# Kernel tuning notes

Measured on AMD Instinct MI355X. Metric: run time of the kernel, lower is better.

## Reference

```python
import jax, jax.numpy as jnp
import numpy as np

NUM_HEADS = 16
D_MODEL = 1024
DEPTH = D_MODEL // NUM_HEADS
B, S = 4, 1024  # q,k seq len = S; v seq len = S-1


def setup_inputs() -> dict:
    key = jax.random.key(0)
    ks = jax.random.split(key, 6)
    scale = 1.0 / np.sqrt(D_MODEL)
    return {
        "v": jax.random.normal(ks[0], (B, S - 1, D_MODEL), dtype=jnp.float32),
        "k": jax.random.normal(ks[1], (B, S, D_MODEL), dtype=jnp.float32),
        "q": jax.random.normal(ks[2], (B, S, D_MODEL), dtype=jnp.float32),
        "mask": jnp.zeros((B, S - 1, S - 1), dtype=jnp.float32),
        "Wv": jax.random.normal(ks[3], (D_MODEL, D_MODEL), dtype=jnp.float32) * scale,
        "bv": jnp.zeros((D_MODEL,), dtype=jnp.float32),
        "Wd": jax.random.normal(ks[4], (D_MODEL, D_MODEL), dtype=jnp.float32) * scale,
        "bd": jnp.zeros((D_MODEL,), dtype=jnp.float32),
    }


def _split_heads(x):
    # (B, T, d_model) -> (B, H, T, depth)
    b, t, _ = x.shape
    return x.reshape(b, t, NUM_HEADS, DEPTH).transpose(0, 2, 1, 3)


def reference(v, k, q, mask, Wv, bv, Wd, bd):
    # 3-D q/k path: qq=q, kk=k (q_layers/k_layers/wq/wk unused)
    vv = v @ Wv + bv                       # (B, S-1, d_model)
    qh = _split_heads(q)                   # (B, H, S, depth)
    kh = _split_heads(k)                   # (B, H, S, depth)
    vh = _split_heads(vv)                  # (B, H, S-1, depth)

    scores = jnp.einsum('bhqd,bhkd->bhqk', qh, kh)      # (B, H, S, S)
    scores = scores[:, :, 1:, :-1]                      # (B, H, S-1, S-1)
    dk = jnp.asarray(DEPTH, scores.dtype)
    nl = jax.nn.relu(scores / jnp.sqrt(dk))
    nl = nl + mask[:, None, :, :] * (-1e9)
    att = jax.nn.softmax(nl, axis=-1)                   # (B, H, S-1, S-1)

    out = jnp.einsum('bhqk,bhkd->bhqd', att, vh)        # (B, H, S-1, depth)
    out = out.transpose(0, 2, 1, 3).reshape(v.shape[0], -1, D_MODEL)  # (B, S-1, d_model)
    output = out @ Wd + bd
    return output, att
```

## Files before the change

### kernel.cpp

```cpp
#include <hip/hip_runtime.h>
#include <hip/hip_bf16.h>

#define NUM_HEADS 16
#define DM 1024
#define DEPTH 64
#define BB 4
#define SS 1024
#define SL 1023
#define M_ROWS (BB*SL)

typedef __attribute__((ext_vector_type(8))) short short8;
typedef __attribute__((ext_vector_type(4))) float floatx4;

__device__ inline unsigned short f2bf(float f) {
  __hip_bfloat16 hb = __float2bfloat16(f);
  return *reinterpret_cast<unsigned short*>(&hb);
}
__device__ inline short8 ld_frag(const unsigned short* p) {
  return *reinterpret_cast<const short8*>(p);
}

#define GLDS(g, l) __builtin_amdgcn_global_load_lds( \
    (const __attribute__((address_space(1))) void*)(g), \
    (__attribute__((address_space(3))) void*)(l), 16, 0, 0)

__global__ __launch_bounds__(256) void f32_to_bf16_vec(
    const float* __restrict__ in, unsigned short* __restrict__ out, int n8)
{
  int i = blockIdx.x * 256 + threadIdx.x;
  if (i >= n8) return;
  const float4 f0 = ((const float4*)in)[(size_t)i * 2];
  const float4 f1 = ((const float4*)in)[(size_t)i * 2 + 1];
  unsigned short t[8];
  t[0]=f2bf(f0.x); t[1]=f2bf(f0.y); t[2]=f2bf(f0.z); t[3]=f2bf(f0.w);
  t[4]=f2bf(f1.x); t[5]=f2bf(f1.y); t[6]=f2bf(f1.z); t[7]=f2bf(f1.w);
  ((uint4*)out)[i] = *(uint4*)t;
}

__global__ __launch_bounds__(256) void transpose_to_bf16(
    const float* __restrict__ W, unsigned short* __restrict__ WT)
{
  __shared__ unsigned short tile[64][72];
  const int tid = threadIdx.x;
  const int k0 = blockIdx.y * 64, n0 = blockIdx.x * 64;
  {
    const int kl = tid >> 2, nc = (tid & 3) * 16;
    const float* src = W + (size_t)(k0 + kl) * DM + n0 + nc;
    #pragma unroll
    for (int j = 0; j < 16; j += 4) {
      float4 f = *(const float4*)(src + j);
      tile[nc + j + 0][kl] = f2bf(f.x);
      tile[nc + j + 1][kl] = f2bf(f.y);
      tile[nc + j + 2][kl] = f2bf(f.z);
      tile[nc + j + 3][kl] = f2bf(f.w);
    }
  }
  __syncthreads();
  {
    const int nl = tid >> 2, kc = (tid & 3) * 16;
    unsigned short tmp[16];
    #pragma unroll
    for (int j = 0; j < 16; j++) tmp[j] = tile[nl][kc + j];
    unsigned short* dst = WT + (size_t)(n0 + nl) * DM + k0 + kc;
    *(uint4*)&dst[0] = *(uint4*)&tmp[0];
    *(uint4*)&dst[8] = *(uint4*)&tmp[8];
  }
}

template <bool OUT_BF16>
__global__ __launch_bounds__(256) void gemm_bt(
    const unsigned short* __restrict__ A,
    const unsigned short* __restrict__ BT,
    const float* __restrict__ bias,
    void* __restrict__ Cv, int M)
{
  constexpr int BM = 64, BN = 128, BK = 32;
  __shared__ __align__(16) unsigned short As[2][BM * BK];
  __shared__ __align__(16) unsigned short Bs[2][BN * BK];

  const int tid = threadIdx.x;
  const int w = tid >> 6, lane = tid & 63, q4 = lane >> 4, l16 = lane & 15;
  const int wm = w >> 1, wn = w & 1;
  const int rb = blockIdx.y * BM;
  const int cb = blockIdx.x * BN;

  const int a_row = tid >> 2;
  const int a_slot = (tid & 3) ^ ((a_row >> 1) & 3);
  int a_grow = rb + a_row; if (a_grow >= M) a_grow = M - 1;
  const unsigned short* a_src = A + (size_t)a_grow * DM + a_slot * 8;
  const int b_row0 = tid >> 2;
  const int b_row1 = 64 + (tid >> 2);
  const int b_slot0 = (tid & 3) ^ ((b_row0 >> 1) & 3);
  const int b_slot1 = (tid & 3) ^ ((b_row1 >> 1) & 3);
  const unsigned short* b_src0 = BT + (size_t)(cb + b_row0) * DM + b_slot0 * 8;
  const unsigned short* b_src1 = BT + (size_t)(cb + b_row1) * DM + b_slot1 * 8;

  int aoff[2], boff[4];
  #pragma unroll
  for (int i = 0; i < 2; i++) {
    int r = wm * 32 + i * 16 + l16;
    aoff[i] = r * BK + ((q4 ^ ((r >> 1) & 3)) * 8);
  }
  #pragma unroll
  for (int j = 0; j < 4; j++) {
    int r = wn * 64 + j * 16 + l16;
    boff[j] = r * BK + ((q4 ^ ((r >> 1) & 3)) * 8);
  }

  floatx4 acc[2][4];
  #pragma unroll
  for (int i = 0; i < 2; i++)
    #pragma unroll
    for (int j = 0; j < 4; j++) acc[i][j] = (floatx4){0.f,0.f,0.f,0.f};

  GLDS(a_src,  &As[0][tid * 8]);
  GLDS(b_src0, &Bs[0][tid * 8]);
  GLDS(b_src1, &Bs[0][2048 + tid * 8]);
  __syncthreads();

  int cur = 0;
  constexpr int NT = DM / BK;
  for (int t = 0; t < NT; ++t) {
    if (t + 1 < NT) {
      const int kn = (t + 1) * BK;
      GLDS(a_src + kn,  &As[cur ^ 1][tid * 8]);
      GLDS(b_src0 + kn, &Bs[cur ^ 1][tid * 8]);
      GLDS(b_src1 + kn, &Bs[cur ^ 1][2048 + tid * 8]);
    }
    short8 af[2], bfr[4];
    #pragma unroll
    for (int i = 0; i < 2; i++) af[i] = ld_frag(&As[cur][aoff[i]]);
    #pragma unroll
    for (int j = 0; j < 4; j++) bfr[j] = ld_frag(&Bs[cur][boff[j]]);
    #pragma unroll
    for (int i = 0; i < 2; i++)
      #pragma unroll
      for (int j = 0; j < 4; j++)
        acc[i][j] = __builtin_amdgcn_mfma_f32_16x16x32_bf16(af[i], bfr[j], acc[i][j], 0, 0, 0);
    __syncthreads();
    cur ^= 1;
  }

  #pragma unroll
  for (int j = 0; j < 4; j++) {
    int col = cb + wn * 64 + j * 16 + l16;
    float bb = bias[col];
    #pragma unroll
    for (int i = 0; i < 2; i++) {
      #pragma unroll
      for (int r = 0; r < 4; r++) {
        int m = rb + wm * 32 + i * 16 + q4 * 4 + r;
        if (m < M) {
          float val = acc[i][j][r] + bb;
          if (OUT_BF16) ((unsigned short*)Cv)[(size_t)m * DM + col] = f2bf(val);
          else          ((float*)Cv)[(size_t)m * DM + col] = val;
        }
      }
    }
  }
}

__global__ __launch_bounds__(256) void attn_kernel(
    const float* __restrict__ Q, const float* __restrict__ Kg,
    const float* __restrict__ Mask, const unsigned short* __restrict__ VV,
    float* __restrict__ Att, unsigned short* __restrict__ Out2)
{
  const int qt = blockIdx.x, h = blockIdx.y, b = blockIdx.z;
  const int tid = threadIdx.x;
  const int w = tid >> 6, lane = tid & 63, q4 = lane >> 4, l16 = lane & 15;
  const int qi0 = qt * 64;
  const int qb = w * 16;

  __shared__ unsigned short qsh[64][72];
  __shared__ unsigned short ksh[64][72];
  __shared__ unsigned short vshT[64][72];
  __shared__ unsigned short psh[4][16][72];

  {
    int qr = tid >> 2, d0 = (tid & 3) * 16;
    int qi = qi0 + qr;
    unsigned short tmp[16];
    if (qi < SL) {
      const float* src = Q + ((size_t)b * SS + qi + 1) * DM + h * DEPTH + d0;
      #pragma unroll
      for (int j = 0; j < 16; j += 4) {
        float4 f = *(const float4*)(src + j);
        tmp[j+0]=f2bf(f.x); tmp[j+1]=f2bf(f.y); tmp[j+2]=f2bf(f.z); tmp[j+3]=f2bf(f.w);
      }
    } else {
      #pragma unroll
      for (int j = 0; j < 16; j++) tmp[j] = 0;
    }
    *(uint4*)&qsh[qr][d0]     = *(uint4*)&tmp[0];
    *(uint4*)&qsh[qr][d0 + 8] = *(uint4*)&tmp[8];
  }

  auto stageK = [&](int kt) {
    int kr = tid >> 2, d0 = (tid & 3) * 16;
    int kj = kt * 64 + kr;
    unsigned short tmp[16];
    if (kj < SL) {
      const float* src = Kg + ((size_t)b * SS + kj) * DM + h * DEPTH + d0;
      #pragma unroll
      for (int j = 0; j < 16; j += 4) {
        float4 f = *(const float4*)(src + j);
        tmp[j+0]=f2bf(f.x); tmp[j+1]=f2bf(f.y); tmp[j+2]=f2bf(f.z); tmp[j+3]=f2bf(f.w);
      }
    } else {
      #pragma unroll
      for (int j = 0; j < 16; j++) tmp[j] = 0;
    }
    *(uint4*)&ksh[kr][d0]     = *(uint4*)&tmp[0];
    *(uint4*)&ksh[kr][d0 + 8] = *(uint4*)&tmp[8];
  };

  auto stageV = [&](int kt) {
    int d = tid & 63, k16 = (tid >> 6) * 16;
    unsigned short tmp[16];
    #pragma unroll
    for (int j = 0; j < 16; j++) {
      int kj = kt * 64 + k16 + j;
      tmp[j] = (kj < SL) ? VV[((size_t)b * SL + kj) * DM + h * DEPTH + d] : (unsigned short)0;
    }
    *(uint4*)&vshT[d][k16]     = *(uint4*)&tmp[0];
    *(uint4*)&vshT[d][k16 + 8] = *(uint4*)&tmp[8];
  };

  __syncthreads();

  float rsv[4] = {0.f, 0.f, 0.f, 0.f};
  for (int kt = 0; kt < 16; kt++) {
    __syncthreads();
    stageK(kt);
    __syncthreads();
    #pragma unroll
    for (int nt = 0; nt < 4; nt++) {
      floatx4 s = (floatx4){0.f,0.f,0.f,0.f};
      s = __builtin_amdgcn_mfma_f32_16x16x32_bf16(
            ld_frag(&qsh[qb + l16][q4*8]), ld_frag(&ksh[nt*16 + l16][q4*8]), s, 0,0,0);
      s = __builtin_amdgcn_mfma_f32_16x16x32_bf16(
            ld_frag(&qsh[qb + l16][32 + q4*8]), ld_frag(&ksh[nt*16 + l16][32 + q4*8]), s, 0,0,0);
      int kj = kt * 64 + nt * 16 + l16;
      bool kv = kj < SL;
      int qi_b = qi0 + qb + q4 * 4;
      const float* mp = Mask + ((size_t)b * SL + qi_b) * SL + kj;
      #pragma unroll
      for (int r = 0; r < 4; r++) {
        int qi = qi_b + r;
        float mval = (kv && qi < SL) ? mp[(size_t)r * SL] : 0.f;
        float sv = fmaxf(s[r] * 0.125f, 0.f) + mval * (-1e9f);
        float p = kv ? __expf(sv) : 0.f;
        rsv[r] += p;
      }
    }
  }
  #pragma unroll
  for (int r = 0; r < 4; r++) {
    #pragma unroll
    for (int off = 1; off < 16; off <<= 1) rsv[r] += __shfl_xor(rsv[r], off, 64);
  }
  float inv[4];
  #pragma unroll
  for (int r = 0; r < 4; r++) inv[r] = 1.f / rsv[r];

  floatx4 oacc[4];
  #pragma unroll
  for (int i = 0; i < 4; i++) oacc[i] = (floatx4){0.f,0.f,0.f,0.f};

  for (int kt = 0; kt < 16; kt++) {
    __syncthreads();
    stageK(kt);
    stageV(kt);
    __syncthreads();
    #pragma unroll
    for (int nt = 0; nt < 4; nt++) {
      floatx4 s = (floatx4){0.f,0.f,0.f,0.f};
      s = __builtin_amdgcn_mfma_f32_16x16x32_bf16(
            ld_frag(&qsh[qb + l16][q4*8]), ld_frag(&ksh[nt*16 + l16][q4*8]), s, 0,0,0);
      s = __builtin_amdgcn_mfma_f32_16x16x32_bf16(
            ld_frag(&qsh[qb + l16][32 + q4*8]), ld_frag(&ksh[nt*16 + l16][32 + q4*8]), s, 0,0,0);
      int kj = kt * 64 + nt * 16 + l16;
      bool kv = kj < SL;
      int qi_b = qi0 + qb + q4 * 4;
      const float* mp = Mask + ((size_t)b * SL + qi_b) * SL + kj;
      #pragma unroll
      for (int r = 0; r < 4; r++) {
        int qi = qi_b + r;
        bool qv = qi < SL;
        float mval = (kv && qv) ? mp[(size_t)r * SL] : 0.f;
        float sv = fmaxf(s[r] * 0.125f, 0.f) + mval * (-1e9f);
        float p = kv ? __expf(sv) : 0.f;
        float pn = p * inv[r];
        if (kv && qv)
          Att[(((size_t)(b * NUM_HEADS + h)) * SL + qi) * SL + kj] = pn;
        psh[w][q4 * 4 + r][nt * 16 + l16] = f2bf(pn);
      }
    }
    short8 pa0 = ld_frag(&psh[w][l16][q4 * 8]);
    short8 pa1 = ld_frag(&psh[w][l16][32 + q4 * 8]);
    #pragma unroll
    for (int nt2 = 0; nt2 < 4; nt2++) {
      oacc[nt2] = __builtin_amdgcn_mfma_f32_16x16x32_bf16(
                    pa0, ld_frag(&vshT[nt2*16 + l16][q4*8]), oacc[nt2], 0,0,0);
      oacc[nt2] = __builtin_amdgcn_mfma_f32_16x16x32_bf16(
                    pa1, ld_frag(&vshT[nt2*16 + l16][32 + q4*8]), oacc[nt2], 0,0,0);
    }
  }

  #pragma unroll
  for (int nt2 = 0; nt2 < 4; nt2++) {
    #pragma unroll
    for (int r = 0; r < 4; r++) {
      int qi = qi0 + qb + q4 * 4 + r;
      if (qi < SL)
        Out2[((size_t)b * SL + qi) * DM + h * DEPTH + nt2 * 16 + l16] = f2bf(oacc[nt2][r]);
    }
  }
}

extern "C" void kernel_launch(void* const* d_in, const int* in_sizes, int n_in,
                              void* d_out, int out_size, void* d_ws, size_t ws_size,
                              hipStream_t stream) {
  const float* v    = (const float*)d_in[0];
  const float* k    = (const float*)d_in[1];
  const float* q    = (const float*)d_in[2];
  const float* mask = (const float*)d_in[3];
  const float* Wv   = (const float*)d_in[4];
  const float* bv   = (const float*)d_in[5];
  const float* Wd   = (const float*)d_in[6];
  const float* bd   = (const float*)d_in[7];

  float* out = (float*)d_out;
  float* att = out + (size_t)M_ROWS * DM;
  unsigned short* vv   = (unsigned short*)d_ws;
  unsigned short* out2 = vv + (size_t)M_ROWS * DM;

  unsigned short* WvT = (unsigned short*)att;
  unsigned short* vbf = WvT + (size_t)DM * DM;
  unsigned short* WdT = vv;

  const int n8 = (M_ROWS * DM) / 8;

  f32_to_bf16_vec<<<dim3((n8 + 255) / 256), 256, 0, stream>>>(v, vbf, n8);
  transpose_to_bf16<<<dim3(16, 16), 256, 0, stream>>>(Wv, WvT);
  gemm_bt<true><<<dim3(DM/128, (M_ROWS+63)/64), 256, 0, stream>>>(vbf, WvT, bv, (void*)vv, M_ROWS);
  attn_kernel<<<dim3(16, NUM_HEADS, BB), 256, 0, stream>>>(q, k, mask, vv, att, out2);
  transpose_to_bf16<<<dim3(16, 16), 256, 0, stream>>>(Wd, WdT);
  gemm_bt<false><<<dim3(DM/128, (M_ROWS+63)/64), 256, 0, stream>>>(out2, WdT, bd, (void*)out, M_ROWS);
}
```

Baseline: 667.0 us.

## Double-buffer K in attention, XOR-swizzle LDS, widen GEMM BK, nontemporal stores

The attention kernel now preloads the Q fragments into registers and double-buffers K tiles in LDS, issuing the next tile's global loads before the current compute. Padded LDS arrays are replaced with XOR-swizzled layouts to avoid bank conflicts. The GEMM K-tile grows from 32 to 64 with a matching 8-way swizzle. The attention-probability and fp32 GEMM outputs use nontemporal stores. Together these aim to hide global latency and cut LDS conflicts, at the cost of more registers and LDS, and extra barriers in the second pass.

```diff
diff --git a/kernel.cpp b/kernel.cpp
--- a/kernel.cpp
+++ b/kernel.cpp
@@ -19,6 +19,8 @@
 __device__ inline short8 ld_frag(const unsigned short* p) {
   return *reinterpret_cast<const short8*>(p);
 }
+
+#define SWZ(row, g) (((g) ^ ((row) & 7)))
 
 #define GLDS(g, l) __builtin_amdgcn_global_load_lds( \
     (const __attribute__((address_space(1))) void*)(g), \
@@ -74,7 +76,7 @@
     const float* __restrict__ bias,
     void* __restrict__ Cv, int M)
 {
-  constexpr int BM = 64, BN = 128, BK = 32;
+  constexpr int BM = 64, BN = 128, BK = 64;
   __shared__ __align__(16) unsigned short As[2][BM * BK];
   __shared__ __align__(16) unsigned short Bs[2][BN * BK];
 
@@ -84,28 +86,32 @@
   const int rb = blockIdx.y * BM;
   const int cb = blockIdx.x * BN;
 
-  const int a_row = tid >> 2;
-  const int a_slot = (tid & 3) ^ ((a_row >> 1) & 3);
-  int a_grow = rb + a_row; if (a_grow >= M) a_grow = M - 1;
-  const unsigned short* a_src = A + (size_t)a_grow * DM + a_slot * 8;
-  const int b_row0 = tid >> 2;
-  const int b_row1 = 64 + (tid >> 2);
-  const int b_slot0 = (tid & 3) ^ ((b_row0 >> 1) & 3);
-  const int b_slot1 = (tid & 3) ^ ((b_row1 >> 1) & 3);
-  const unsigned short* b_src0 = BT + (size_t)(cb + b_row0) * DM + b_slot0 * 8;
-  const unsigned short* b_src1 = BT + (size_t)(cb + b_row1) * DM + b_slot1 * 8;
-
-  int aoff[2], boff[4];
-  #pragma unroll
-  for (int i = 0; i < 2; i++) {
-    int r = wm * 32 + i * 16 + l16;
-    aoff[i] = r * BK + ((q4 ^ ((r >> 1) & 3)) * 8);
-  }
-  #pragma unroll
-  for (int j = 0; j < 4; j++) {
-    int r = wn * 64 + j * 16 + l16;
-    boff[j] = r * BK + ((q4 ^ ((r >> 1) & 3)) * 8);
-  }
+  const int srow = tid >> 3;
+  const int lg   = (tid & 7) ^ (srow & 7);
+  int ar0 = rb + srow;       if (ar0 >= M) ar0 = M - 1;
+  int ar1 = rb + 32 + srow;  if (ar1 >= M) ar1 = M - 1;
+  const unsigned short* a_src0 = A + (size_t)ar0 * DM + lg * 8;
+  const unsigned short* a_src1 = A + (size_t)ar1 * DM + lg * 8;
+  const unsigned short* b_src0 = BT + (size_t)(cb      + srow) * DM + lg * 8;
+  const unsigned short* b_src1 = BT + (size_t)(cb + 32 + srow) * DM + lg * 8;
+  const unsigned short* b_src2 = BT + (size_t)(cb + 64 + srow) * DM + lg * 8;
+  const unsigned short* b_src3 = BT + (size_t)(cb + 96 + srow) * DM + lg * 8;
+
+  int aoff[2][2], boff[4][2];
+  #pragma unroll
+  for (int i = 0; i < 2; i++)
+    #pragma unroll
+    for (int hf = 0; hf < 2; hf++) {
+      int r = wm * 32 + i * 16 + l16;
+      aoff[i][hf] = r * BK + SWZ(r, q4 + 4 * hf) * 8;
+    }
+  #pragma unroll
+  for (int j = 0; j < 4; j++)
+    #pragma unroll
+    for (int hf = 0; hf < 2; hf++) {
+      int r = wn * 64 + j * 16 + l16;
+      boff[j][hf] = r * BK + SWZ(r, q4 + 4 * hf) * 8;
+    }
 
   floatx4 acc[2][4];
   #pragma unroll
@@ -113,9 +119,12 @@
     #pragma unroll
     for (int j = 0; j < 4; j++) acc[i][j] = (floatx4){0.f,0.f,0.f,0.f};
 
-  GLDS(a_src,  &As[0][tid * 8]);
+  GLDS(a_src0, &As[0][tid * 8]);
+  GLDS(a_src1, &As[0][2048 + tid * 8]);
   GLDS(b_src0, &Bs[0][tid * 8]);
   GLDS(b_src1, &Bs[0][2048 + tid * 8]);
+  GLDS(b_src2, &Bs[0][4096 + tid * 8]);
+  GLDS(b_src3, &Bs[0][6144 + tid * 8]);
   __syncthreads();
 
   int cur = 0;
@@ -123,20 +132,30 @@
   for (int t = 0; t < NT; ++t) {
     if (t + 1 < NT) {
       const int kn = (t + 1) * BK;
-      GLDS(a_src + kn,  &As[cur ^ 1][tid * 8]);
+      GLDS(a_src0 + kn, &As[cur ^ 1][tid * 8]);
+      GLDS(a_src1 + kn, &As[cur ^ 1][2048 + tid * 8]);
       GLDS(b_src0 + kn, &Bs[cur ^ 1][tid * 8]);
       GLDS(b_src1 + kn, &Bs[cur ^ 1][2048 + tid * 8]);
-    }
-    short8 af[2], bfr[4];
-    #pragma unroll
-    for (int i = 0; i < 2; i++) af[i] = ld_frag(&As[cur][aoff[i]]);
-    #pragma unroll
-    for (int j = 0; j < 4; j++) bfr[j] = ld_frag(&Bs[cur][boff[j]]);
-    #pragma unroll
-    for (int i = 0; i < 2; i++)
-      #pragma unroll
-      for (int j = 0; j < 4; j++)
-        acc[i][j] = __builtin_amdgcn_mfma_f32_16x16x32_bf16(af[i], bfr[j], acc[i][j], 0, 0, 0);
+      GLDS(b_src2 + kn, &Bs[cur ^ 1][4096 + tid * 8]);
+      GLDS(b_src3 + kn, &Bs[cur ^ 1][6144 + tid * 8]);
+    }
+    #pragma unroll
+    for (int hf = 0; hf < 2; hf++) {
+      short8 af0 = ld_frag(&As[cur][aoff[0][hf]]);
+      short8 af1 = ld_frag(&As[cur][aoff[1][hf]]);
+      short8 bf0 = ld_frag(&Bs[cur][boff[0][hf]]);
+      short8 bf1 = ld_frag(&Bs[cur][boff[1][hf]]);
+      short8 bf2 = ld_frag(&Bs[cur][boff[2][hf]]);
+      short8 bf3 = ld_frag(&Bs[cur][boff[3][hf]]);
+      acc[0][0] = __builtin_amdgcn_mfma_f32_16x16x32_bf16(af0, bf0, acc[0][0], 0,0,0);
+      acc[0][1] = __builtin_amdgcn_mfma_f32_16x16x32_bf16(af0, bf1, acc[0][1], 0,0,0);
+      acc[0][2] = __builtin_amdgcn_mfma_f32_16x16x32_bf16(af0, bf2, acc[0][2], 0,0,0);
+      acc[0][3] = __builtin_amdgcn_mfma_f32_16x16x32_bf16(af0, bf3, acc[0][3], 0,0,0);
+      acc[1][0] = __builtin_amdgcn_mfma_f32_16x16x32_bf16(af1, bf0, acc[1][0], 0,0,0);
+      acc[1][1] = __builtin_amdgcn_mfma_f32_16x16x32_bf16(af1, bf1, acc[1][1], 0,0,0);
+      acc[1][2] = __builtin_amdgcn_mfma_f32_16x16x32_bf16(af1, bf2, acc[1][2], 0,0,0);
+      acc[1][3] = __builtin_amdgcn_mfma_f32_16x16x32_bf16(af1, bf3, acc[1][3], 0,0,0);
+    }
     __syncthreads();
     cur ^= 1;
   }
@@ -153,7 +172,7 @@
         if (m < M) {
           float val = acc[i][j][r] + bb;
           if (OUT_BF16) ((unsigned short*)Cv)[(size_t)m * DM + col] = f2bf(val);
-          else          ((float*)Cv)[(size_t)m * DM + col] = val;
+          else __builtin_nontemporal_store(val, &((float*)Cv)[(size_t)m * DM + col]);
         }
       }
     }
@@ -171,88 +190,99 @@
   const int qi0 = qt * 64;
   const int qb = w * 16;
 
-  __shared__ unsigned short qsh[64][72];
-  __shared__ unsigned short ksh[64][72];
-  __shared__ unsigned short vshT[64][72];
-  __shared__ unsigned short psh[4][16][72];
+  __shared__ __align__(16) unsigned short qsh[64][64];
+  __shared__ __align__(16) unsigned short ksh[2][64][64];
+  __shared__ __align__(16) unsigned short vshT[64][64];
+  __shared__ __align__(16) unsigned short psh[4][16][64];
 
   {
-    int qr = tid >> 2, d0 = (tid & 3) * 16;
-    int qi = qi0 + qr;
-    unsigned short tmp[16];
+    const int qr = tid >> 2, c = tid & 3;
+    const int qi = qi0 + qr;
+    unsigned short t0[8], t1[8];
     if (qi < SL) {
-      const float* src = Q + ((size_t)b * SS + qi + 1) * DM + h * DEPTH + d0;
-      #pragma unroll
-      for (int j = 0; j < 16; j += 4) {
-        float4 f = *(const float4*)(src + j);
-        tmp[j+0]=f2bf(f.x); tmp[j+1]=f2bf(f.y); tmp[j+2]=f2bf(f.z); tmp[j+3]=f2bf(f.w);
-      }
+      const float* src = Q + ((size_t)b * SS + qi + 1) * DM + h * DEPTH + c * 16;
+      float4 f0 = ((const float4*)src)[0], f1 = ((const float4*)src)[1];
+      float4 f2 = ((const float4*)src)[2], f3 = ((const float4*)src)[3];
+      t0[0]=f2bf(f0.x); t0[1]=f2bf(f0.y); t0[2]=f2bf(f0.z); t0[3]=f2bf(f0.w);
+      t0[4]=f2bf(f1.x); t0[5]=f2bf(f1.y); t0[6]=f2bf(f1.z); t0[7]=f2bf(f1.w);
+      t1[0]=f2bf(f2.x); t1[1]=f2bf(f2.y); t1[2]=f2bf(f2.z); t1[3]=f2bf(f2.w);
+      t1[4]=f2bf(f3.x); t1[5]=f2bf(f3.y); t1[6]=f2bf(f3.z); t1[7]=f2bf(f3.w);
     } else {
       #pragma unroll
-      for (int j = 0; j < 16; j++) tmp[j] = 0;
-    }
-    *(uint4*)&qsh[qr][d0]     = *(uint4*)&tmp[0];
-    *(uint4*)&qsh[qr][d0 + 8] = *(uint4*)&tmp[8];
-  }
-
-  auto stageK = [&](int kt) {
-    int kr = tid >> 2, d0 = (tid & 3) * 16;
-    int kj = kt * 64 + kr;
-    unsigned short tmp[16];
+      for (int j = 0; j < 8; j++) { t0[j] = 0; t1[j] = 0; }
+    }
+    *(uint4*)&qsh[qr][SWZ(qr, 2*c)     * 8] = *(uint4*)t0;
+    *(uint4*)&qsh[qr][SWZ(qr, 2*c + 1) * 8] = *(uint4*)t1;
+  }
+
+  const int kr = tid >> 2, kc = tid & 3;
+  auto loadK = [&](int kt, float4* f) {
+    const int kj = kt * 64 + kr;
     if (kj < SL) {
-      const float* src = Kg + ((size_t)b * SS + kj) * DM + h * DEPTH + d0;
-      #pragma unroll
-      for (int j = 0; j < 16; j += 4) {
-        float4 f = *(const float4*)(src + j);
-        tmp[j+0]=f2bf(f.x); tmp[j+1]=f2bf(f.y); tmp[j+2]=f2bf(f.z); tmp[j+3]=f2bf(f.w);
-      }
+      const float* src = Kg + ((size_t)b * SS + kj) * DM + h * DEPTH + kc * 16;
+      f[0] = ((const float4*)src)[0]; f[1] = ((const float4*)src)[1];
+      f[2] = ((const float4*)src)[2]; f[3] = ((const float4*)src)[3];
     } else {
-      #pragma unroll
-      for (int j = 0; j < 16; j++) tmp[j] = 0;
-    }
-    *(uint4*)&ksh[kr][d0]     = *(uint4*)&tmp[0];
-    *(uint4*)&ksh[kr][d0 + 8] = *(uint4*)&tmp[8];
+      f[0] = f[1] = f[2] = f[3] = (float4){0.f,0.f,0.f,0.f};
+    }
   };
-
-  auto stageV = [&](int kt) {
-    int d = tid & 63, k16 = (tid >> 6) * 16;
-    unsigned short tmp[16];
+  auto writeK = [&](int buf, const float4* f) {
+    unsigned short t0[8], t1[8];
+    t0[0]=f2bf(f[0].x); t0[1]=f2bf(f[0].y); t0[2]=f2bf(f[0].z); t0[3]=f2bf(f[0].w);
+    t0[4]=f2bf(f[1].x); t0[5]=f2bf(f[1].y); t0[6]=f2bf(f[1].z); t0[7]=f2bf(f[1].w);
+    t1[0]=f2bf(f[2].x); t1[1]=f2bf(f[2].y); t1[2]=f2bf(f[2].z); t1[3]=f2bf(f[2].w);
+    t1[4]=f2bf(f[3].x); t1[5]=f2bf(f[3].y); t1[6]=f2bf(f[3].z); t1[7]=f2bf(f[3].w);
+    *(uint4*)&ksh[buf][kr][SWZ(kr, 2*kc)     * 8] = *(uint4*)t0;
+    *(uint4*)&ksh[buf][kr][SWZ(kr, 2*kc + 1) * 8] = *(uint4*)t1;
+  };
+  const int vd = tid & 63, vg = (tid >> 6) * 2;
+  auto loadV = [&](int kt, unsigned short* t) {
     #pragma unroll
     for (int j = 0; j < 16; j++) {
-      int kj = kt * 64 + k16 + j;
-      tmp[j] = (kj < SL) ? VV[((size_t)b * SL + kj) * DM + h * DEPTH + d] : (unsigned short)0;
-    }
-    *(uint4*)&vshT[d][k16]     = *(uint4*)&tmp[0];
-    *(uint4*)&vshT[d][k16 + 8] = *(uint4*)&tmp[8];
+      int kj = kt * 64 + vg * 8 + j;
+      t[j] = (kj < SL) ? VV[((size_t)b * SL + kj) * DM + h * DEPTH + vd] : (unsigned short)0;
+    }
   };
-
+  auto writeV = [&](const unsigned short* t) {
+    *(uint4*)&vshT[vd][SWZ(vd, vg)     * 8] = *(uint4*)&t[0];
+    *(uint4*)&vshT[vd][SWZ(vd, vg + 1) * 8] = *(uint4*)&t[8];
+  };
+
+  float4 kreg[4];
+  loadK(0, kreg);
+  writeK(0, kreg);
   __syncthreads();
+
+  const int qrow = qb + l16;
+  const short8 qf0 = ld_frag(&qsh[qrow][SWZ(qrow, q4)     * 8]);
+  const short8 qf1 = ld_frag(&qsh[qrow][SWZ(qrow, 4 + q4) * 8]);
+  const int qi_b = qi0 + qb + q4 * 4;
 
   float rsv[4] = {0.f, 0.f, 0.f, 0.f};
   for (int kt = 0; kt < 16; kt++) {
-    __syncthreads();
-    stageK(kt);
-    __syncthreads();
+    const int cur = kt & 1;
+    if (kt < 15) loadK(kt + 1, kreg);
     #pragma unroll
     for (int nt = 0; nt < 4; nt++) {
+      const int krow = nt * 16 + l16;
       floatx4 s = (floatx4){0.f,0.f,0.f,0.f};
       s = __builtin_amdgcn_mfma_f32_16x16x32_bf16(
-            ld_frag(&qsh[qb + l16][q4*8]), ld_frag(&ksh[nt*16 + l16][q4*8]), s, 0,0,0);
+            qf0, ld_frag(&ksh[cur][krow][SWZ(krow, q4)     * 8]), s, 0,0,0);
       s = __builtin_amdgcn_mfma_f32_16x16x32_bf16(
-            ld_frag(&qsh[qb + l16][32 + q4*8]), ld_frag(&ksh[nt*16 + l16][32 + q4*8]), s, 0,0,0);
+            qf1, ld_frag(&ksh[cur][krow][SWZ(krow, 4 + q4) * 8]), s, 0,0,0);
       int kj = kt * 64 + nt * 16 + l16;
       bool kv = kj < SL;
-      int qi_b = qi0 + qb + q4 * 4;
       const float* mp = Mask + ((size_t)b * SL + qi_b) * SL + kj;
       #pragma unroll
       for (int r = 0; r < 4; r++) {
         int qi = qi_b + r;
         float mval = (kv && qi < SL) ? mp[(size_t)r * SL] : 0.f;
         float sv = fmaxf(s[r] * 0.125f, 0.f) + mval * (-1e9f);
-        float p = kv ? __expf(sv) : 0.f;
-        rsv[r] += p;
+        rsv[r] += kv ? __expf(sv) : 0.f;
       }
     }
+    if (kt < 15) writeK(cur ^ 1, kreg);
+    __syncthreads();
   }
   #pragma unroll
   for (int r = 0; r < 4; r++) {
@@ -267,22 +297,27 @@
   #pragma unroll
   for (int i = 0; i < 4; i++) oacc[i] = (floatx4){0.f,0.f,0.f,0.f};
 
+  loadK(0, kreg);
+  writeK(0, kreg);
+  __syncthreads();
+
   for (int kt = 0; kt < 16; kt++) {
-    __syncthreads();
-    stageK(kt);
-    stageV(kt);
-    __syncthreads();
+    const int cur = kt & 1;
+    unsigned short vreg[16];
+    loadV(kt, vreg);
+    if (kt < 15) loadK(kt + 1, kreg);
     #pragma unroll
     for (int nt = 0; nt < 4; nt++) {
+      const int krow = nt * 16 + l16;
       floatx4 s = (floatx4){0.f,0.f,0.f,0.f};
       s = __builtin_amdgcn_mfma_f32_16x16x32_bf16(
-            ld_frag(&qsh[qb + l16][q4*8]), ld_frag(&ksh[nt*16 + l16][q4*8]), s, 0,0,0);
+            qf0, ld_frag(&ksh[cur][krow][SWZ(krow, q4)     * 8]), s, 0,0,0);
       s = __builtin_amdgcn_mfma_f32_16x16x32_bf16(
-            ld_frag(&qsh[qb + l16][32 + q4*8]), ld_frag(&ksh[nt*16 + l16][32 + q4*8]), s, 0,0,0);
+            qf1, ld_frag(&ksh[cur][krow][SWZ(krow, 4 + q4) * 8]), s, 0,0,0);
       int kj = kt * 64 + nt * 16 + l16;
       bool kv = kj < SL;
-      int qi_b = qi0 + qb + q4 * 4;
       const float* mp = Mask + ((size_t)b * SL + qi_b) * SL + kj;
+      const int pg = nt * 2 + (l16 >> 3), pc = l16 & 7;
       #pragma unroll
       for (int r = 0; r < 4; r++) {
         int qi = qi_b + r;
@@ -292,19 +327,26 @@
         float p = kv ? __expf(sv) : 0.f;
         float pn = p * inv[r];
         if (kv && qv)
-          Att[(((size_t)(b * NUM_HEADS + h)) * SL + qi) * SL + kj] = pn;
-        psh[w][q4 * 4 + r][nt * 16 + l16] = f2bf(pn);
+          __builtin_nontemporal_store(pn,
+              &Att[(((size_t)(b * NUM_HEADS + h)) * SL + qi) * SL + kj]);
+        const int prow = q4 * 4 + r;
+        psh[w][prow][SWZ(prow, pg) * 8 + pc] = f2bf(pn);
       }
     }
-    short8 pa0 = ld_frag(&psh[w][l16][q4 * 8]);
-    short8 pa1 = ld_frag(&psh[w][l16][32 + q4 * 8]);
+    writeV(vreg);
+    if (kt < 15) writeK(cur ^ 1, kreg);
+    short8 pa0 = ld_frag(&psh[w][l16][SWZ(l16, q4)     * 8]);
+    short8 pa1 = ld_frag(&psh[w][l16][SWZ(l16, 4 + q4) * 8]);
+    __syncthreads();
     #pragma unroll
     for (int nt2 = 0; nt2 < 4; nt2++) {
+      const int vrow = nt2 * 16 + l16;
       oacc[nt2] = __builtin_amdgcn_mfma_f32_16x16x32_bf16(
-                    pa0, ld_frag(&vshT[nt2*16 + l16][q4*8]), oacc[nt2], 0,0,0);
+                    pa0, ld_frag(&vshT[vrow][SWZ(vrow, q4)     * 8]), oacc[nt2], 0,0,0);
       oacc[nt2] = __builtin_amdgcn_mfma_f32_16x16x32_bf16(
-                    pa1, ld_frag(&vshT[nt2*16 + l16][32 + q4*8]), oacc[nt2], 0,0,0);
-    }
+                    pa1, ld_frag(&vshT[vrow][SWZ(vrow, 4 + q4) * 8]), oacc[nt2], 0,0,0);
+    }
+    __syncthreads();
   }
 
   #pragma unroll
```

After: 845.7 us. +26.8%, slower.
